# Optimization experiments

Measured on AMD Instinct MI355X. Metric: run time of the kernel, lower is better.

## Reference

```python
import jax, jax.numpy as jnp
import numpy as np

B, DIM, NH, NB = 4, 1024, 4, 2
HD = DIM // NH


def _pe_enc(coords, gauss):
    # SAM PositionEmbeddingRandom._pe_encoding: coords in [0,1], shape (...,2)
    c = 2.0 * coords - 1.0
    c = c @ gauss                      # (..., DIM//2)
    c = (2.0 * np.pi) * c
    return jnp.concatenate([jnp.sin(c), jnp.cos(c)], axis=-1)  # (..., DIM)


def _ln(x, w, b):
    m = jnp.mean(x, axis=-1, keepdims=True)
    v = jnp.mean((x - m) ** 2, axis=-1, keepdims=True)
    return (x - m) * jax.lax.rsqrt(v + 1e-5) * w + b


def _attn(x, qkv_w, qkv_b, pw, pb):
    Bb, N, C = x.shape
    qkv = (x @ qkv_w + qkv_b).reshape(Bb, N, 3, NH, HD)
    q, k, v = qkv[:, :, 0], qkv[:, :, 1], qkv[:, :, 2]        # (B,N,H,D)
    a = jnp.einsum('bnhd,bmhd->bhnm', q * (HD ** -0.5), k)
    a = jax.nn.softmax(a, axis=-1)
    o = jnp.einsum('bhnm,bmhd->bnhd', a, v).reshape(Bb, N, C)
    return o @ pw + pb


def _block(i, first, x, x_pe, ctx, ctx_pe, p):
    # pe='normal', use_sep=True, init_values=0 -> LayerScale is identity
    if first:
        x = x + x_pe
        ctx = ctx + ctx_pe
    xl, cl = x.shape[1], ctx.shape[1]
    x = jnp.concatenate([x, p['sep'][i], ctx], axis=1)
    x = x + _attn(_ln(x, p['ln1_w'][i], p['ln1_b'][i]),
                  p['qkv_w'][i], p['qkv_b'][i], p['proj_w'][i], p['proj_b'][i])
    h = _ln(x, p['ln2_w'][i], p['ln2_b'][i])
    x = x + (jax.nn.gelu(h @ p['mlp_w1'][i] + p['mlp_b1'][i], approximate=False)
             @ p['mlp_w2'][i] + p['mlp_b2'][i])
    return x[:, :xl], x[:, xl + 1:xl + 1 + cl]


def _forward(image_embeddings, prompt_depth, gauss, d2f_w1, d2f_b1, d2f_w2, d2f_b2,
             p, idx_list, patch_h, patch_w):
    Hm, Wm = prompt_depth.shape[2], prompt_depth.shape[3]
    ys = (jnp.arange(patch_h, dtype=jnp.float32) + 0.5) / patch_h
    xs = (jnp.arange(patch_w, dtype=jnp.float32) + 0.5) / patch_w
    xx, yy = jnp.meshgrid(xs, ys)                              # (ph, pw)
    query_pe = _pe_enc(jnp.stack([xx, yy], axis=-1), gauss).reshape(1, -1, DIM)
    outs = []
    for b in range(image_embeddings.shape[0]):
        rows, cols = idx_list[b]
        if rows.size == 0:
            outs.append(image_embeddings[b:b + 1])
            continue
        # nonzero order: (row, col); module indexes pe with [col, row] = (x, y)
        pos = jnp.stack([(jnp.asarray(cols, dtype=jnp.float32) + 0.5) / Wm,
                         (jnp.asarray(rows, dtype=jnp.float32) + 0.5) / Hm], axis=-1)
        prompt_pe = _pe_enc(pos, gauss)[None]                  # (1, P, DIM)
        d = prompt_depth[b, 0][rows, cols][:, None]            # (P, 1)
        prompt = (jax.nn.gelu(d @ d2f_w1 + d2f_b1, approximate=False)
                  @ d2f_w2 + d2f_b2)[None]                     # (1, P, DIM)
        query = image_embeddings[b:b + 1]
        for i in range(NB):
            query, prompt = _block(i, i == 0, query, query_pe, prompt, prompt_pe, p)
        outs.append(query)
    return jnp.concatenate(outs, axis=0)


def setup_inputs() -> dict:
    key = jax.random.key(0)
    ks = jax.random.split(key, 12)
    f = jnp.float32
    rn = lambda k, s, sc=0.02: jax.random.normal(k, s, f) * sc
    return dict(
        image_embeddings=jax.random.normal(ks[0], (B, 1024, DIM), f),
        prompt_depth=jax.random.uniform(ks[1], (B, 1, 48, 48), dtype=f),
        prompt_mask=jax.random.randint(ks[2], (B, 1, 48, 48), 0, 2).astype(jnp.int32),
        patch_h=32, patch_w=32,
        gauss=jax.random.normal(ks[3], (2, DIM // 2), f),
        d2f_w1=rn(ks[4], (1, DIM // 2)), d2f_b1=jnp.zeros((DIM // 2,), f),
        d2f_w2=rn(ks[5], (DIM // 2, DIM)), d2f_b2=jnp.zeros((DIM,), f),
        sep=rn(ks[6], (NB, 1, 1, DIM), 1.0),
        ln1_w=jnp.ones((NB, DIM), f), ln1_b=jnp.zeros((NB, DIM), f),
        qkv_w=rn(ks[7], (NB, DIM, 3 * DIM)), qkv_b=jnp.zeros((NB, 3 * DIM), f),
        proj_w=rn(ks[8], (NB, DIM, DIM)), proj_b=jnp.zeros((NB, DIM), f),
        ln2_w=jnp.ones((NB, DIM), f), ln2_b=jnp.zeros((NB, DIM), f),
        mlp_w1=rn(ks[9], (NB, DIM, 4 * DIM)), mlp_b1=jnp.zeros((NB, 4 * DIM), f),
        mlp_w2=rn(ks[10], (NB, 4 * DIM, DIM)), mlp_b2=jnp.zeros((NB, DIM), f),
    )


def reference(image_embeddings, prompt_depth, prompt_mask, patch_h, patch_w,
              gauss, d2f_w1, d2f_b1, d2f_w2, d2f_b2, sep,
              ln1_w, ln1_b, qkv_w, qkv_b, proj_w, proj_b,
              ln2_w, ln2_b, mlp_w1, mlp_b1, mlp_w2, mlp_b2):
    m = np.asarray(prompt_mask)
    idx = [np.nonzero(m[b, 0] > 0) for b in range(m.shape[0])]
    p = dict(sep=sep, ln1_w=ln1_w, ln1_b=ln1_b, qkv_w=qkv_w, qkv_b=qkv_b,
             proj_w=proj_w, proj_b=proj_b, ln2_w=ln2_w, ln2_b=ln2_b,
             mlp_w1=mlp_w1, mlp_b1=mlp_b1, mlp_w2=mlp_w2, mlp_b2=mlp_b2)
    return _forward(image_embeddings, prompt_depth, gauss,
                    d2f_w1, d2f_b1, d2f_w2, d2f_b2, p, idx, int(patch_h), int(patch_w))
```

## Files before the change

### kernel.cpp

```cpp
#include <hip/hip_runtime.h>
#include <math.h>

#define NBATCH 4
#define DIM    1024
#define NHEAD  4
#define HD     256
#define NQ     1024
#define MASKN  2304
#define NMAX   3329
#define TWO_PI 6.283185307179586f

typedef unsigned short bf16_t;
typedef short bf16x8 __attribute__((ext_vector_type(8)));
typedef float f32x4  __attribute__((ext_vector_type(4)));

__device__ __forceinline__ float gelu_exact(float x) {
    return 0.5f * x * (1.0f + erff(x * 0.70710678118654752f));
}
__device__ __forceinline__ float bf2f(bf16_t h) {
    return __uint_as_float((unsigned)h << 16);
}
__device__ __forceinline__ bf16_t f2bf(float f) {
    unsigned u = __float_as_uint(f);
    return (bf16_t)((u + 0x7FFFu + ((u >> 16) & 1u)) >> 16);
}

__global__ __launch_bounds__(256)
void k_compact(const int* __restrict__ mask, int* __restrict__ cnt, int* __restrict__ pidx) {
    int b = blockIdx.x;
    __shared__ int sc;
    if (threadIdx.x == 0) sc = 0;
    __syncthreads();
    for (int c = threadIdx.x; c < MASKN; c += blockDim.x)
        if (mask[b * MASKN + c] > 0) {
            int p = atomicAdd(&sc, 1);
            pidx[b * MASKN + p] = c;
        }
    __syncthreads();
    if (threadIdx.x == 0) cnt[b] = sc;
}

__global__ __launch_bounds__(256)
void k_zerobias(float* __restrict__ z) {
    z[blockIdx.x * 256 + threadIdx.x] = 0.f;
}

__global__ __launch_bounds__(256)
void k_init_query(const float* __restrict__ emb, const float* __restrict__ gauss,
                  float* __restrict__ X) {
    int b = blockIdx.y, n = blockIdx.x, t = threadIdx.x;
    float fx = 2.0f * (((n & 31) + 0.5f) / 32.0f) - 1.0f;
    float fy = 2.0f * (((n >> 5) + 0.5f) / 32.0f) - 1.0f;
    const float* e = emb + ((size_t)b * NQ + n) * DIM;
    float* x = X + ((size_t)b * NMAX + n) * DIM;
    for (int d = t; d < 512; d += 256) {
        float ang = TWO_PI * (fx * gauss[d] + fy * gauss[512 + d]);
        float sn, cs; sincosf(ang, &sn, &cs);
        x[d]       = e[d] + sn;
        x[d + 512] = e[d + 512] + cs;
    }
}

__global__ __launch_bounds__(256)
void k_prompt_h(const float* __restrict__ depth, const float* __restrict__ w1,
                const float* __restrict__ b1, const int* __restrict__ cnt,
                const int* __restrict__ pidx, bf16_t* __restrict__ Hp) {
    int b = blockIdx.y, s = blockIdx.x, t = threadIdx.x;
    bf16_t* hp = Hp + ((size_t)b * MASKN + s) * 512;
    if (s >= cnt[b]) { hp[t] = 0; hp[t + 256] = 0; return; }
    int cell = pidx[b * MASKN + s];
    float d = depth[b * MASKN + cell];
    for (int j = t; j < 512; j += 256)
        hp[j] = f2bf(gelu_exact(fmaf(d, w1[j], b1[j])));
}

__global__ __launch_bounds__(256)
void k_pe_prompt(const float* __restrict__ gauss, const int* __restrict__ cnt,
                 const int* __restrict__ pidx, float* __restrict__ X) {
    int b = blockIdx.y, s = blockIdx.x, t = threadIdx.x;
    if (s >= cnt[b]) return;
    int cell = pidx[b * MASKN + s];
    int r = cell / 48, c = cell % 48;
    float fx = 2.0f * ((c + 0.5f) / 48.0f) - 1.0f;
    float fy = 2.0f * ((r + 0.5f) / 48.0f) - 1.0f;
    float* x = X + ((size_t)b * NMAX + 1025 + s) * DIM;
    for (int d = t; d < 512; d += 256) {
        float ang = TWO_PI * (fx * gauss[d] + fy * gauss[512 + d]);
        float sn, cs; sincosf(ang, &sn, &cs);
        x[d]       += sn;
        x[d + 512] += cs;
    }
}

__global__ __launch_bounds__(256)
void k_sep(float* __restrict__ X, const float* __restrict__ sep) {
    int b = blockIdx.x, t = threadIdx.x;
    float* x = X + ((size_t)b * NMAX + 1024) * DIM;
    *(float4*)&x[t * 4] = *(const float4*)&sep[t * 4];
}

__global__ __launch_bounds__(256)
void k_ln(const float* __restrict__ X, bf16_t* __restrict__ Xn,
          const float* __restrict__ w, const float* __restrict__ bb,
          const int* __restrict__ cnt) {
    int b = blockIdx.y, n = blockIdx.x;
    int Nb = 1025 + cnt[b];
    if (n >= Nb) return;
    int t = threadIdx.x;
    const float* x = X + ((size_t)b * NMAX + n) * DIM;
    float4 v = *(const float4*)&x[t * 4];
    float s = v.x + v.y + v.z + v.w;
    float q = v.x * v.x + v.y * v.y + v.z * v.z + v.w * v.w;
    #pragma unroll
    for (int off = 32; off > 0; off >>= 1) {
        s += __shfl_xor(s, off);
        q += __shfl_xor(q, off);
    }
    __shared__ float ss[4], sq[4];
    int wave = t >> 6, lane = t & 63;
    if (lane == 0) { ss[wave] = s; sq[wave] = q; }
    __syncthreads();
    s = ss[0] + ss[1] + ss[2] + ss[3];
    q = sq[0] + sq[1] + sq[2] + sq[3];
    float mean = s * (1.0f / DIM);
    float var  = q * (1.0f / DIM) - mean * mean;
    float rstd = 1.0f / sqrtf(var + 1e-5f);
    float4 ww = *(const float4*)&w[t * 4];
    float4 b4 = *(const float4*)&bb[t * 4];
    ushort4 o;
    o.x = f2bf((v.x - mean) * rstd * ww.x + b4.x);
    o.y = f2bf((v.y - mean) * rstd * ww.y + b4.y);
    o.z = f2bf((v.z - mean) * rstd * ww.z + b4.z);
    o.w = f2bf((v.w - mean) * rstd * ww.w + b4.w);
    *(ushort4*)&(Xn + ((size_t)b * NMAX + n) * DIM)[t * 4] = o;
}

template <int EPI, typename OutT>
__global__ __launch_bounds__(256)
void k_gemm_mfma(const bf16_t* __restrict__ A, size_t bsA, int ldA,
                 const float* __restrict__ W, int ldW, const float* __restrict__ bias,
                 OutT* __restrict__ Out, size_t bsO, int ldO,
                 int K, const int* __restrict__ cnt, int bound_add, int rows_phys) {
    int b = blockIdx.z;
    int bound = cnt[b] + bound_add;
    int tr = blockIdx.y * 128;
    if (tr >= bound) return;
    int tc = blockIdx.x * 128;

    __shared__ bf16_t As[128][40];
    __shared__ bf16_t Bs[128][40];

    int tid  = threadIdx.x;
    int wave = tid >> 6, lane = tid & 63;
    int quad = lane >> 4, l16 = lane & 15;
    int wr = (wave >> 1) * 64, wc = (wave & 1) * 64;

    f32x4 acc[4][4];
    #pragma unroll
    for (int mi = 0; mi < 4; ++mi)
        #pragma unroll
        for (int ni = 0; ni < 4; ++ni)
            acc[mi][ni] = (f32x4){0.f, 0.f, 0.f, 0.f};

    const bf16_t* Ab = A + (size_t)b * bsA;
    int ar = tid >> 1;
    int ac = (tid & 1) * 16;
    int bn  = tid & 127;
    int bkc = tid >> 7;

    for (int k0 = 0; k0 < K; k0 += 32) {
        __syncthreads();
        {
            int row = tr + ar;
            bf16x8 v0 = (bf16x8){0,0,0,0,0,0,0,0};
            bf16x8 v1 = (bf16x8){0,0,0,0,0,0,0,0};
            if (row < rows_phys) {
                const bf16_t* ap = Ab + (size_t)row * ldA + k0 + ac;
                v0 = *(const bf16x8*)ap;
                v1 = *(const bf16x8*)(ap + 8);
            }
            *(bf16x8*)&As[ar][ac]     = v0;
            *(bf16x8*)&As[ar][ac + 8] = v1;
        }
        #pragma unroll
        for (int c0 = 0; c0 < 2; ++c0) {
            int kk = (bkc + c0 * 2) * 8;
            const float* wp = W + (size_t)(k0 + kk) * ldW + tc + bn;
            bf16_t tmp[8];
            #pragma unroll
            for (int j = 0; j < 8; ++j)
                tmp[j] = f2bf(wp[(size_t)j * ldW]);
            *(bf16x8*)&Bs[bn][kk] = *(bf16x8*)tmp;
        }
        __syncthreads();

        bf16x8 af[4], bfr[4];
        #pragma unroll
        for (int mi = 0; mi < 4; ++mi)
            af[mi] = *(const bf16x8*)&As[wr + mi * 16 + l16][quad * 8];
        #pragma unroll
        for (int ni = 0; ni < 4; ++ni)
            bfr[ni] = *(const bf16x8*)&Bs[wc + ni * 16 + l16][quad * 8];
        #pragma unroll
        for (int mi = 0; mi < 4; ++mi)
            #pragma unroll
            for (int ni = 0; ni < 4; ++ni)
                acc[mi][ni] = __builtin_amdgcn_mfma_f32_16x16x32_bf16(
                    af[mi], bfr[ni], acc[mi][ni], 0, 0, 0);
    }

    OutT* Ob = Out + (size_t)b * bsO;
    #pragma unroll
    for (int ni = 0; ni < 4; ++ni) {
        int col = tc + wc + ni * 16 + l16;
        float bs = bias[col];
        #pragma unroll
        for (int mi = 0; mi < 4; ++mi) {
            int row0 = tr + wr + mi * 16 + quad * 4;
            #pragma unroll
            for (int r = 0; r < 4; ++r) {
                int row = row0 + r;
                if (row >= rows_phys) continue;
                float v = acc[mi][ni][r] + bs;
                if (EPI == 1) v = gelu_exact(v);
                OutT* op = Ob + (size_t)row * ldO + col;
                if (EPI == 2) v += *(const float*)op;
                if (sizeof(OutT) == 2) *(bf16_t*)op = f2bf(v);
                else                   *(float*)op  = v;
            }
        }
    }
}

__global__ __launch_bounds__(256)
void k_attn_mfma(const bf16_t* __restrict__ QKV, bf16_t* __restrict__ O,
                 const int* __restrict__ cnt) {
    int b = blockIdx.z, h = blockIdx.y;
    int Nb = 1025 + cnt[b];
    int qbase = blockIdx.x * 64;
    if (qbase >= Nb) return;

    __shared__ bf16_t Kt[32][264];
    __shared__ bf16_t Vt[256][40];
    __shared__ bf16_t Pt[4][16][40];

    int tid  = threadIdx.x;
    int wave = tid >> 6, lane = tid & 63;
    int quad = lane >> 4, l16 = lane & 15;

    int qrow  = qbase + wave * 16 + l16;
    int qrowc = qrow < NMAX ? qrow : NMAX - 1;
    const bf16_t* Qp = QKV + (size_t)b * NMAX * 3072 + (size_t)qrowc * 3072 + h * HD;
    bf16x8 qf[8];
    #pragma unroll
    for (int c = 0; c < 8; ++c)
        qf[c] = *(const bf16x8*)(Qp + c * 32 + quad * 8);

    f32x4 Oacc[16];
    #pragma unroll
    for (int n = 0; n < 16; ++n) Oacc[n] = (f32x4){0.f, 0.f, 0.f, 0.f};
    float l[4] = {0.f, 0.f, 0.f, 0.f};

    const bf16_t* Kg = QKV + (size_t)b * NMAX * 3072 + 1024 + h * HD;
    const bf16_t* Vg = QKV + (size_t)b * NMAX * 3072 + 2048 + h * HD;

    int krow_s = tid >> 3;
    int kd_s   = (tid & 7) * 8;
    int vd_s   = (tid >> 3) * 8;
    int vr_s   = (tid & 7) * 4;

    for (int kt = 0; kt < Nb; kt += 32) {
        __syncthreads();
        #pragma unroll
        for (int i = 0; i < 4; ++i) {
            int gk = kt + krow_s;
            int d  = kd_s + i * 64;
            bf16x8 v = (bf16x8){0,0,0,0,0,0,0,0};
            if (gk < Nb) v = *(const bf16x8*)(Kg + (size_t)gk * 3072 + d);
            *(bf16x8*)&Kt[krow_s][d] = v;
        }
        {
            bf16x8 vv[4];
            #pragma unroll
            for (int r = 0; r < 4; ++r) {
                int gk = kt + vr_s + r;
                vv[r] = (bf16x8){0,0,0,0,0,0,0,0};
                if (gk < Nb) vv[r] = *(const bf16x8*)(Vg + (size_t)gk * 3072 + vd_s);
            }
            #pragma unroll
            for (int j = 0; j < 8; ++j) {
                ushort4 pk;
                pk.x = (unsigned short)vv[0][j];
                pk.y = (unsigned short)vv[1][j];
                pk.z = (unsigned short)vv[2][j];
                pk.w = (unsigned short)vv[3][j];
                *(ushort4*)&Vt[vd_s + j][vr_s] = pk;
            }
        }
        __syncthreads();

        f32x4 c0 = (f32x4){0.f,0.f,0.f,0.f}, c1 = (f32x4){0.f,0.f,0.f,0.f};
        #pragma unroll
        for (int c = 0; c < 8; ++c) {
            bf16x8 kb0 = *(const bf16x8*)&Kt[l16     ][c * 32 + quad * 8];
            bf16x8 kb1 = *(const bf16x8*)&Kt[l16 + 16][c * 32 + quad * 8];
            c0 = __builtin_amdgcn_mfma_f32_16x16x32_bf16(qf[c], kb0, c0, 0, 0, 0);
            c1 = __builtin_amdgcn_mfma_f32_16x16x32_bf16(qf[c], kb1, c1, 0, 0, 0);
        }
        float ls[4];
        #pragma unroll
        for (int r = 0; r < 4; ++r) {
            float p0 = (kt + l16      < Nb) ? __expf(c0[r] * 0.0625f) : 0.f;
            float p1 = (kt + 16 + l16 < Nb) ? __expf(c1[r] * 0.0625f) : 0.f;
            Pt[wave][quad * 4 + r][l16]      = f2bf(p0);
            Pt[wave][quad * 4 + r][l16 + 16] = f2bf(p1);
            ls[r] = p0 + p1;
        }
        #pragma unroll
        for (int off = 1; off < 16; off <<= 1)
            #pragma unroll
            for (int r = 0; r < 4; ++r)
                ls[r] += __shfl_xor(ls[r], off);
        #pragma unroll
        for (int r = 0; r < 4; ++r) l[r] += ls[r];

        bf16x8 pa = *(const bf16x8*)&Pt[wave][l16][quad * 8];
        #pragma unroll
        for (int n = 0; n < 16; ++n) {
            bf16x8 vb = *(const bf16x8*)&Vt[n * 16 + l16][quad * 8];
            Oacc[n] = __builtin_amdgcn_mfma_f32_16x16x32_bf16(pa, vb, Oacc[n], 0, 0, 0);
        }
    }

    float inv[4];
    #pragma unroll
    for (int r = 0; r < 4; ++r) inv[r] = 1.0f / l[r];
    bf16_t* Op = O + (size_t)b * NMAX * DIM + h * HD;
    #pragma unroll
    for (int r = 0; r < 4; ++r) {
        int row = qbase + wave * 16 + quad * 4 + r;
        if (row < Nb) {
            bf16_t* op = Op + (size_t)row * DIM;
            #pragma unroll
            for (int n = 0; n < 16; ++n)
                op[n * 16 + l16] = f2bf(Oacc[n][r] * inv[r]);
        }
    }
}

__global__ __launch_bounds__(256)
void k_out(const float* __restrict__ X, const float* __restrict__ emb,
           const int* __restrict__ cnt, float* __restrict__ out) {
    int b = blockIdx.y, n = blockIdx.x, t = threadIdx.x;
    const float* s = (cnt[b] > 0) ? X + ((size_t)b * NMAX + n) * DIM
                                  : emb + ((size_t)b * NQ + n) * DIM;
    *(float4*)&out[((size_t)b * NQ + n) * DIM + t * 4] = *(const float4*)&s[t * 4];
}

extern "C" void kernel_launch(void* const* d_in, const int* in_sizes, int n_in,
                              void* d_out, int out_size, void* d_ws, size_t ws_size,
                              hipStream_t stream) {
    const float* emb    = (const float*)d_in[0];
    const float* depth  = (const float*)d_in[1];
    const int*   mask   = (const int*)d_in[2];
    const float* gauss  = (const float*)d_in[5];
    const float* d2f_w1 = (const float*)d_in[6];
    const float* d2f_b1 = (const float*)d_in[7];
    const float* d2f_w2 = (const float*)d_in[8];
    const float* d2f_b2 = (const float*)d_in[9];
    const float* sep    = (const float*)d_in[10];
    const float* ln1_w  = (const float*)d_in[11];
    const float* ln1_b  = (const float*)d_in[12];
    const float* qkv_w  = (const float*)d_in[13];
    const float* qkv_b  = (const float*)d_in[14];
    const float* proj_w = (const float*)d_in[15];
    const float* proj_b = (const float*)d_in[16];
    const float* ln2_w  = (const float*)d_in[17];
    const float* ln2_b  = (const float*)d_in[18];
    const float* mlp_w1 = (const float*)d_in[19];
    const float* mlp_b1 = (const float*)d_in[20];
    const float* mlp_w2 = (const float*)d_in[21];
    const float* mlp_b2 = (const float*)d_in[22];
    float* out = (float*)d_out;

    char* wsb = (char*)d_ws;
    int*    cnt   = (int*)wsb;
    int*    pidx  = (int*)(wsb + 256);
    float*  zbias = (float*)(wsb + 37120);
    float*  X     = (float*)(wsb + 41216);
    bf16_t* Xn    = (bf16_t*)(wsb + 41216 + (size_t)NBATCH * NMAX * DIM * 4);
    bf16_t* Qb    = (bf16_t*)(wsb + 41216 + (size_t)NBATCH * NMAX * DIM * 6);
    if (ws_size < (size_t)163668224) return;

    k_compact<<<NBATCH, 256, 0, stream>>>(mask, cnt, pidx);
    k_zerobias<<<4, 256, 0, stream>>>(zbias);
    k_init_query<<<dim3(NQ, NBATCH), 256, 0, stream>>>(emb, gauss, X);
    k_prompt_h<<<dim3(MASKN, NBATCH), 256, 0, stream>>>(depth, d2f_w1, d2f_b1, cnt, pidx, Qb);
    k_gemm_mfma<0, float><<<dim3(8, 18, NBATCH), 256, 0, stream>>>(
        Qb, (size_t)MASKN * 512, 512, d2f_w2, DIM, d2f_b2,
        X + (size_t)1025 * DIM, (size_t)NMAX * DIM, DIM, 512, cnt, 0, MASKN);
    k_pe_prompt<<<dim3(MASKN, NBATCH), 256, 0, stream>>>(gauss, cnt, pidx, X);

    for (int i = 0; i < 2; ++i) {
        k_sep<<<NBATCH, 256, 0, stream>>>(X, sep + (size_t)i * DIM);
        k_ln<<<dim3(NMAX, NBATCH), 256, 0, stream>>>(X, Xn, ln1_w + i * DIM, ln1_b + i * DIM, cnt);
        k_gemm_mfma<0, bf16_t><<<dim3(24, 27, NBATCH), 256, 0, stream>>>(
            Xn, (size_t)NMAX * DIM, DIM,
            qkv_w + (size_t)i * DIM * 3072, 3072, qkv_b + (size_t)i * 3072,
            Qb, (size_t)NMAX * 3072, 3072, DIM, cnt, 1025, NMAX);
        k_attn_mfma<<<dim3(53, NHEAD, NBATCH), 256, 0, stream>>>(Qb, Xn, cnt);
        k_gemm_mfma<2, float><<<dim3(8, 27, NBATCH), 256, 0, stream>>>(
            Xn, (size_t)NMAX * DIM, DIM,
            proj_w + (size_t)i * DIM * DIM, DIM, proj_b + (size_t)i * DIM,
            X, (size_t)NMAX * DIM, DIM, DIM, cnt, 1025, NMAX);
        k_ln<<<dim3(NMAX, NBATCH), 256, 0, stream>>>(X, Xn, ln2_w + i * DIM, ln2_b + i * DIM, cnt);
        for (int c = 0; c < 2; ++c) {
            k_gemm_mfma<1, bf16_t><<<dim3(16, 27, NBATCH), 256, 0, stream>>>(
                Xn, (size_t)NMAX * DIM, DIM,
                mlp_w1 + (size_t)i * DIM * 4096 + c * 2048, 4096,
                mlp_b1 + (size_t)i * 4096 + c * 2048,
                Qb, (size_t)NMAX * 2048, 2048, DIM, cnt, 1025, NMAX);
            k_gemm_mfma<2, float><<<dim3(8, 27, NBATCH), 256, 0, stream>>>(
                Qb, (size_t)NMAX * 2048, 2048,
                mlp_w2 + (size_t)i * 4096 * DIM + (size_t)c * 2048 * DIM, DIM,
                (c == 0) ? (mlp_b2 + (size_t)i * DIM) : zbias,
                X, (size_t)NMAX * DIM, DIM, 2048, cnt, 1025, NMAX);
        }
    }

    k_out<<<dim3(NQ, NBATCH), 256, 0, stream>>>(X, emb, cnt, out);
    (void)in_sizes; (void)n_in; (void)out_size;
}
```

Before: 1.980 ms.

## Pre-transpose weights to bf16 K-major and widen GEMM K-tile to 64

Adds a transpose kernel that converts each fp32 weight matrix to a bf16 N-by-K layout once per block. The GEMM then loads B tiles with contiguous 16-byte vector loads instead of strided scalar fp32 loads with an in-loop conversion. The GEMM K step also goes from 32 to 64, halving the number of barriers per tile. The cost is extra transpose launches plus a weight pass each call, and roughly double the LDS per block.

Measured after the change: 1.720 ms. 1.15x faster.

```diff
diff --git a/kernel.cpp b/kernel.cpp
--- a/kernel.cpp
+++ b/kernel.cpp
@@ -43,6 +43,28 @@
 __global__ __launch_bounds__(256)
 void k_zerobias(float* __restrict__ z) {
     z[blockIdx.x * 256 + threadIdx.x] = 0.f;
+}
+
+__global__ __launch_bounds__(256)
+void k_wt(const float* __restrict__ W, bf16_t* __restrict__ Wt, int K, int N) {
+    __shared__ float T[64][65];
+    int n0 = blockIdx.x * 64, k0 = blockIdx.y * 64;
+    int tid = threadIdx.x;
+    int lr = tid >> 4, lc = (tid & 15) * 4;
+    #pragma unroll
+    for (int i = 0; i < 4; ++i) {
+        float4 v = *(const float4*)&W[(size_t)(k0 + lr + i * 16) * N + n0 + lc];
+        T[lr + i * 16][lc + 0] = v.x; T[lr + i * 16][lc + 1] = v.y;
+        T[lr + i * 16][lc + 2] = v.z; T[lr + i * 16][lc + 3] = v.w;
+    }
+    __syncthreads();
+    int on = tid >> 2, ok = (tid & 3) * 16;
+    bf16_t tmp[16];
+    #pragma unroll
+    for (int j = 0; j < 16; ++j) tmp[j] = f2bf(T[ok + j][on]);
+    bf16_t* op = Wt + (size_t)(n0 + on) * K + k0 + ok;
+    *(bf16x8*)op       = *(bf16x8*)&tmp[0];
+    *(bf16x8*)(op + 8) = *(bf16x8*)&tmp[8];
 }
 
 __global__ __launch_bounds__(256)
@@ -137,18 +159,18 @@
 
 template <int EPI, typename OutT>
 __global__ __launch_bounds__(256)
-void k_gemm_mfma(const bf16_t* __restrict__ A, size_t bsA, int ldA,
-                 const float* __restrict__ W, int ldW, const float* __restrict__ bias,
-                 OutT* __restrict__ Out, size_t bsO, int ldO,
-                 int K, const int* __restrict__ cnt, int bound_add, int rows_phys) {
+void k_gemm_bt(const bf16_t* __restrict__ A, size_t bsA, int ldA,
+               const bf16_t* __restrict__ Wt, int ldWt, const float* __restrict__ bias,
+               OutT* __restrict__ Out, size_t bsO, int ldO,
+               int K, const int* __restrict__ cnt, int bound_add, int rows_phys) {
     int b = blockIdx.z;
     int bound = cnt[b] + bound_add;
     int tr = blockIdx.y * 128;
     if (tr >= bound) return;
     int tc = blockIdx.x * 128;
 
-    __shared__ bf16_t As[128][40];
-    __shared__ bf16_t Bs[128][40];
+    __shared__ bf16_t As[128][72];
+    __shared__ bf16_t Bs[128][72];
 
     int tid  = threadIdx.x;
     int wave = tid >> 6, lane = tid & 63;
@@ -163,50 +185,49 @@
             acc[mi][ni] = (f32x4){0.f, 0.f, 0.f, 0.f};
 
     const bf16_t* Ab = A + (size_t)b * bsA;
-    int ar = tid >> 1;
-    int ac = (tid & 1) * 16;
-    int bn  = tid & 127;
-    int bkc = tid >> 7;
-
-    for (int k0 = 0; k0 < K; k0 += 32) {
+    int sr = tid >> 1;
+    int sc = (tid & 1) * 32;
+
+    for (int k0 = 0; k0 < K; k0 += 64) {
         __syncthreads();
         {
-            int row = tr + ar;
-            bf16x8 v0 = (bf16x8){0,0,0,0,0,0,0,0};
-            bf16x8 v1 = (bf16x8){0,0,0,0,0,0,0,0};
+            int row = tr + sr;
+            bf16x8 v[4];
+            #pragma unroll
+            for (int j = 0; j < 4; ++j) v[j] = (bf16x8){0,0,0,0,0,0,0,0};
             if (row < rows_phys) {
-                const bf16_t* ap = Ab + (size_t)row * ldA + k0 + ac;
-                v0 = *(const bf16x8*)ap;
-                v1 = *(const bf16x8*)(ap + 8);
+                const bf16_t* ap = Ab + (size_t)row * ldA + k0 + sc;
+                #pragma unroll
+                for (int j = 0; j < 4; ++j) v[j] = *(const bf16x8*)(ap + j * 8);
             }
-            *(bf16x8*)&As[ar][ac]     = v0;
-            *(bf16x8*)&As[ar][ac + 8] = v1;
-        }
-        #pragma unroll
-        for (int c0 = 0; c0 < 2; ++c0) {
-            int kk = (bkc + c0 * 2) * 8;
-            const float* wp = W + (size_t)(k0 + kk) * ldW + tc + bn;
-            bf16_t tmp[8];
-            #pragma unroll
-            for (int j = 0; j < 8; ++j)
-                tmp[j] = f2bf(wp[(size_t)j * ldW]);
-            *(bf16x8*)&Bs[bn][kk] = *(bf16x8*)tmp;
+            #pragma unroll
+            for (int j = 0; j < 4; ++j) *(bf16x8*)&As[sr][sc + j * 8] = v[j];
+        }
+        {
+            const bf16_t* bp = Wt + (size_t)(tc + sr) * ldWt + k0 + sc;
+            #pragma unroll
+            for (int j = 0; j < 4; ++j)
+                *(bf16x8*)&Bs[sr][sc + j * 8] = *(const bf16x8*)(bp + j * 8);
         }
         __syncthreads();
 
-        bf16x8 af[4], bfr[4];
-        #pragma unroll
-        for (int mi = 0; mi < 4; ++mi)
-            af[mi] = *(const bf16x8*)&As[wr + mi * 16 + l16][quad * 8];
-        #pragma unroll
-        for (int ni = 0; ni < 4; ++ni)
-            bfr[ni] = *(const bf16x8*)&Bs[wc + ni * 16 + l16][quad * 8];
-        #pragma unroll
-        for (int mi = 0; mi < 4; ++mi)
+        #pragma unroll
+        for (int half = 0; half < 2; ++half) {
+            int ko = half * 32 + quad * 8;
+            bf16x8 af[4], bfr[4];
+            #pragma unroll
+            for (int mi = 0; mi < 4; ++mi)
+                af[mi] = *(const bf16x8*)&As[wr + mi * 16 + l16][ko];
             #pragma unroll
             for (int ni = 0; ni < 4; ++ni)
-                acc[mi][ni] = __builtin_amdgcn_mfma_f32_16x16x32_bf16(
-                    af[mi], bfr[ni], acc[mi][ni], 0, 0, 0);
+                bfr[ni] = *(const bf16x8*)&Bs[wc + ni * 16 + l16][ko];
+            #pragma unroll
+            for (int mi = 0; mi < 4; ++mi)
+                #pragma unroll
+                for (int ni = 0; ni < 4; ++ni)
+                    acc[mi][ni] = __builtin_amdgcn_mfma_f32_16x16x32_bf16(
+                        af[mi], bfr[ni], acc[mi][ni], 0, 0, 0);
+        }
     }
 
     OutT* Ob = Out + (size_t)b * bsO;
@@ -388,41 +409,49 @@
     int*    pidx  = (int*)(wsb + 256);
     float*  zbias = (float*)(wsb + 37120);
     float*  X     = (float*)(wsb + 41216);
-    bf16_t* Xn    = (bf16_t*)(wsb + 41216 + (size_t)NBATCH * NMAX * DIM * 4);
-    bf16_t* Qb    = (bf16_t*)(wsb + 41216 + (size_t)NBATCH * NMAX * DIM * 6);
-    if (ws_size < (size_t)163668224) return;
+    bf16_t* Xn    = (bf16_t*)(wsb + 54583552);
+    bf16_t* Qb    = (bf16_t*)(wsb + 81854720);
+    bf16_t* Wt_qkv = (bf16_t*)(wsb + 163668224);
+    bf16_t* Wt_proj= (bf16_t*)(wsb + 169959680);
+    bf16_t* Wt_m1  = (bf16_t*)(wsb + 172056832);
+    bf16_t* Wt_m2  = (bf16_t*)(wsb + 180445440);
+    if (ws_size < (size_t)188834048) return;
 
     k_compact<<<NBATCH, 256, 0, stream>>>(mask, cnt, pidx);
     k_zerobias<<<4, 256, 0, stream>>>(zbias);
     k_init_query<<<dim3(NQ, NBATCH), 256, 0, stream>>>(emb, gauss, X);
     k_prompt_h<<<dim3(MASKN, NBATCH), 256, 0, stream>>>(depth, d2f_w1, d2f_b1, cnt, pidx, Qb);
-    k_gemm_mfma<0, float><<<dim3(8, 18, NBATCH), 256, 0, stream>>>(
-        Qb, (size_t)MASKN * 512, 512, d2f_w2, DIM, d2f_b2,
+    k_wt<<<dim3(16, 8), 256, 0, stream>>>(d2f_w2, Wt_qkv, 512, DIM);
+    k_gemm_bt<0, float><<<dim3(8, 18, NBATCH), 256, 0, stream>>>(
+        Qb, (size_t)MASKN * 512, 512, Wt_qkv, 512, d2f_b2,
         X + (size_t)1025 * DIM, (size_t)NMAX * DIM, DIM, 512, cnt, 0, MASKN);
     k_pe_prompt<<<dim3(MASKN, NBATCH), 256, 0, stream>>>(gauss, cnt, pidx, X);
 
     for (int i = 0; i < 2; ++i) {
+        k_wt<<<dim3(48, 16), 256, 0, stream>>>(qkv_w  + (size_t)i * DIM * 3072, Wt_qkv,  DIM, 3072);
+        k_wt<<<dim3(16, 16), 256, 0, stream>>>(proj_w + (size_t)i * DIM * DIM,  Wt_proj, DIM, DIM);
+        k_wt<<<dim3(64, 16), 256, 0, stream>>>(mlp_w1 + (size_t)i * DIM * 4096, Wt_m1,   DIM, 4096);
+        k_wt<<<dim3(16, 64), 256, 0, stream>>>(mlp_w2 + (size_t)i * 4096 * DIM, Wt_m2,   4096, DIM);
+
         k_sep<<<NBATCH, 256, 0, stream>>>(X, sep + (size_t)i * DIM);
         k_ln<<<dim3(NMAX, NBATCH), 256, 0, stream>>>(X, Xn, ln1_w + i * DIM, ln1_b + i * DIM, cnt);
-        k_gemm_mfma<0, bf16_t><<<dim3(24, 27, NBATCH), 256, 0, stream>>>(
-            Xn, (size_t)NMAX * DIM, DIM,
-            qkv_w + (size_t)i * DIM * 3072, 3072, qkv_b + (size_t)i * 3072,
+        k_gemm_bt<0, bf16_t><<<dim3(24, 27, NBATCH), 256, 0, stream>>>(
+            Xn, (size_t)NMAX * DIM, DIM, Wt_qkv, DIM, qkv_b + (size_t)i * 3072,
             Qb, (size_t)NMAX * 3072, 3072, DIM, cnt, 1025, NMAX);
         k_attn_mfma<<<dim3(53, NHEAD, NBATCH), 256, 0, stream>>>(Qb, Xn, cnt);
-        k_gemm_mfma<2, float><<<dim3(8, 27, NBATCH), 256, 0, stream>>>(
-            Xn, (size_t)NMAX * DIM, DIM,
-            proj_w + (size_t)i * DIM * DIM, DIM, proj_b + (size_t)i * DIM,
+        k_gemm_bt<2, float><<<dim3(8, 27, NBATCH), 256, 0, stream>>>(
+            Xn, (size_t)NMAX * DIM, DIM, Wt_proj, DIM, proj_b + (size_t)i * DIM,
             X, (size_t)NMAX * DIM, DIM, DIM, cnt, 1025, NMAX);
         k_ln<<<dim3(NMAX, NBATCH), 256, 0, stream>>>(X, Xn, ln2_w + i * DIM, ln2_b + i * DIM, cnt);
         for (int c = 0; c < 2; ++c) {
-            k_gemm_mfma<1, bf16_t><<<dim3(16, 27, NBATCH), 256, 0, stream>>>(
+            k_gemm_bt<1, bf16_t><<<dim3(16, 27, NBATCH), 256, 0, stream>>>(
                 Xn, (size_t)NMAX * DIM, DIM,
-                mlp_w1 + (size_t)i * DIM * 4096 + c * 2048, 4096,
+                Wt_m1 + (size_t)c * 2048 * DIM, DIM,
                 mlp_b1 + (size_t)i * 4096 + c * 2048,
                 Qb, (size_t)NMAX * 2048, 2048, DIM, cnt, 1025, NMAX);
-            k_gemm_mfma<2, float><<<dim3(8, 27, NBATCH), 256, 0, stream>>>(
+            k_gemm_bt<2, float><<<dim3(8, 27, NBATCH), 256, 0, stream>>>(
                 Qb, (size_t)NMAX * 2048, 2048,
-                mlp_w2 + (size_t)i * 4096 * DIM + (size_t)c * 2048 * DIM, DIM,
+                Wt_m2 + (size_t)c * 2048, 4096,
                 (c == 0) ? (mlp_b2 + (size_t)i * DIM) : zbias,
                 X, (size_t)NMAX * DIM, DIM, 2048, cnt, 1025, NMAX);
         }
```
